# Kernel optimization log

Measured on AMD Instinct MI355X. Metric: run time of the kernel, lower is better.

The kernel has to match this reference:

```python
import jax, jax.numpy as jnp
import numpy as np

DIM = 24
HID = 256
N = 4096
NUM_LO = DIM * (DIM - 1) // 2  # 276
NEG = -0.01  # slope used in the hand-written Jacobians (source uses -0.01, NOT the fwd leaky slope 0.01; faithful)


def _linear_params(key, out_dim, in_dim):
    kw, kb = jax.random.split(key)
    s = 1.0 / np.sqrt(in_dim)
    W = jax.random.uniform(kw, (out_dim, in_dim), jnp.float32, -s, s)
    b = jax.random.uniform(kb, (out_dim,), jnp.float32, -s, s)
    return W, b


def setup_inputs() -> dict:
    key = jax.random.key(0)
    k = jax.random.split(key, 7)
    W1, b1 = _linear_params(k[0], HID, DIM)
    W2, b2 = _linear_params(k[1], HID, HID)
    WG, bG = _linear_params(k[2], DIM, HID)
    WLd, bLd = _linear_params(k[3], DIM, HID)
    WLo, bLo = _linear_params(k[4], NUM_LO, HID)
    q = jax.random.normal(k[5], (N, DIM), jnp.float32)
    q_dot = jax.random.normal(k[6], (N, DIM), jnp.float32)
    return {"q": q, "q_dot": q_dot, "W1": W1, "b1": b1, "W2": W2, "b2": b2,
            "WG": WG, "bG": bG, "WLd": WLd, "bLd": bLd, "WLo": WLo, "bLo": bLo}


def _forward(q, q_dot, W1, b1, W2, b2, WG, bG, WLd, bLd, WLo, bLo):
    n, d = q.shape
    tr, tc = np.tril_indices(d, -1)  # row-major strict-lower order == torch mask-flatten order
    di = np.arange(d)
    # MLP trunk (torch leaky_relu default slope 0.01)
    h1 = jax.nn.leaky_relu(q @ W1.T + b1)                       # [n,HID]
    h2 = jax.nn.leaky_relu(h1 @ W2.T + b2)                      # [n,HID]
    h3 = h2 @ WLd.T + bLd                                       # [n,d]
    g = h2 @ WG.T + bG                                          # [n,d]
    Ld = jax.nn.softplus(h3)                                    # [n,d]
    Lo = h2 @ WLo.T + bLo                                       # [n,NUM_LO]
    # Lower-triangular L (diag_embed(Ld) + masked strict-lower fill)
    L = jnp.zeros((n, d, d), q.dtype).at[:, tr, tc].set(Lo).at[:, di, di].set(Ld)
    # Hand-written Jacobian chain; diag_embed(v)@W == v[:,:,None]*W (direct elementwise scaling)
    dR1 = jnp.where(h1 > 0, 1.0, NEG)
    J1 = dR1[:, :, None] * W1                                    # dh1/dq  [n,HID,d]
    dR2 = jnp.where(h2 > 0, 1.0, NEG)
    J2 = dR2[:, :, None] * jnp.einsum('ij,njd->nid', W2, J1)     # dh2/dq  [n,HID,d]
    sig = jax.nn.sigmoid(h3)
    dld_dq = sig[:, :, None] * jnp.einsum('ij,njd->nid', WLd, J2)  # [n,d,d]
    dlo_dq = jnp.einsum('oj,njd->nod', WLo, J2)                  # [n,NUM_LO,d]
    dld_dt = jnp.einsum('nid,nd->ni', dld_dq, q_dot)             # [n,d]
    dlo_dt = jnp.einsum('nod,nd->no', dlo_dq, q_dot)             # [n,NUM_LO]
    dL_dt = jnp.zeros((n, d, d), q.dtype).at[:, tr, tc].set(dlo_dt).at[:, di, di].set(dld_dt)
    # 4D assembly: torch does L[L==1] = dlo_dq.view(-1), which reinterprets the (lo, q_idx)
    # flat buffer in (q_idx, tril_pos) order -> plain reshape replicates that exactly.
    vals = dlo_dq.reshape(n, d, NUM_LO)
    dld_dq_p = dld_dq.transpose(0, 2, 1)                         # [n, d_q, d_ld]
    dL_dq = jnp.zeros((n, d, d, d), q.dtype).at[:, :, tr, tc].set(vals).at[:, :, di, di].set(dld_dq_p)
    eye = jnp.eye(d, dtype=q.dtype)
    M = L @ L.transpose(0, 2, 1) + 1e-9 * eye
    dM_dt = L @ dL_dt.transpose(0, 2, 1) + dL_dt @ L.transpose(0, 2, 1)
    # Quadratic term. torch: q_dot.repeat(d,1)/L.repeat(d,1,1) index as (i % n) while
    # dL_dq.view(n*d,d,d) indexes as (i // d, i % d) -> replicate exactly (faithful).
    idx = jnp.arange(n * d) % n
    qd_r = q_dot[idx]                                            # [n*d, d]
    L_r = L[idx]                                                 # [n*d, d, d]
    dL_i = dL_dq.reshape(n * d, d, d)
    S = dL_i @ L_r.transpose(0, 2, 1) + L_r @ dL_i.transpose(0, 2, 1)
    quad = jnp.einsum('bi,bij,bj->b', qd_r, S, qd_r).reshape(n, d)
    c = jnp.einsum('nij,nj->ni', dM_dt, q_dot) - 0.5 * quad
    return M, c, g


def reference(q, q_dot, W1, b1, W2, b2, WG, bG, WLd, bLd, WLo, bLo):
    return _forward(q, q_dot, W1, b1, W2, b2, WG, bG, WLd, bLd, WLo, bLo)
```

## Files before the change

### kernel.cpp

```cpp
#include <hip/hip_runtime.h>
#include <math.h>

#define DIM 24
#define HID 256
#define NLO 276
#define NSAMP 4096
#define C_OFF 2359296
#define G_OFF 2457600

#define OFF_W2FH 0
#define OFF_W2FL 32768
#define OFF_WEFH 65536
#define OFF_WEFL 106496
#define OFF_W1H16 147456
#define OFF_W1L16 151552
#define OFF_W2H16 155648
#define OFF_W2L16 188416
#define OFF_WHH16 221184
#define OFF_WHL16 264192
#define OFF_REC  307200
#define REC_STRIDE 364

typedef __attribute__((ext_vector_type(8))) short bf16x8;
typedef __attribute__((ext_vector_type(8))) _Float16 f16x8;
typedef __attribute__((ext_vector_type(4))) float f32x4;

__device__ __forceinline__ float leaky(float x){ return x > 0.f ? x : 0.01f*x; }
__device__ __forceinline__ unsigned short f2b(float f){
  unsigned u = __float_as_uint(f);
  return (unsigned short)((u + 0x7FFFu + ((u >> 16) & 1u)) >> 16);
}
__device__ __forceinline__ float b2f(unsigned short h){ return __uint_as_float(((unsigned)h) << 16); }
__device__ __forceinline__ void f2h2(float v, unsigned short* hi, unsigned short* lo){
  _Float16 h = (_Float16)v;
  _Float16 l = (_Float16)((v - (float)h) * 4096.f);
  *hi = *(unsigned short*)&h; *lo = *(unsigned short*)&l;
}

__global__ __launch_bounds__(256) void k0_prep(
    const float* __restrict__ W1, const float* __restrict__ W2,
    const float* __restrict__ WG, const float* __restrict__ WLd,
    const float* __restrict__ WLo, float* __restrict__ ws)
{
  const int tid = blockIdx.x*256 + threadIdx.x;
  const int nth = gridDim.x*256;
  unsigned short* W2FH = (unsigned short*)(ws + OFF_W2FH);
  unsigned short* W2FL = (unsigned short*)(ws + OFF_W2FL);
  for (int e = tid; e < 65536; e += nth){
    int j=e&7, l=(e>>3)&63, kb=(e>>9)&7, mt=e>>12;
    int m = mt*16+(l&15), k = kb*32+((l>>4)&3)*8+j;
    float v = W2[m*256+k];
    unsigned short h = f2b(v);
    W2FH[e]=h; W2FL[e]=f2b(v-b2f(h));
  }
  unsigned short* WEFH = (unsigned short*)(ws + OFF_WEFH);
  unsigned short* WEFL = (unsigned short*)(ws + OFF_WEFL);
  for (int e = tid; e < 81920; e += nth){
    int j=e&7, l=(e>>3)&63, kb=(e>>9)&7, mt=e>>12;
    int r = mt*16+(l&15), k = kb*32+((l>>4)&3)*8+j;
    float v = 0.f;
    if (r < 24) v = WLd[r*256+k]; else if (r < 300) v = WLo[(r-24)*256+k];
    unsigned short h = f2b(v);
    WEFH[e]=h; WEFL[e]=f2b(v-b2f(h));
  }
  unsigned short* W1H = (unsigned short*)(ws + OFF_W1H16);
  unsigned short* W1L = (unsigned short*)(ws + OFF_W1L16);
  for (int e = tid; e < 8192; e += nth){
    int j=e&7, l=(e>>3)&63, mt=e>>9;
    int m = mt*16+(l&15), k = ((l>>4)&3)*8+j;
    float v = (k < 24) ? W1[m*24+k] : 0.f;
    f2h2(v, &W1H[e], &W1L[e]);
  }
  unsigned short* W2H = (unsigned short*)(ws + OFF_W2H16);
  unsigned short* W2L = (unsigned short*)(ws + OFF_W2L16);
  for (int e = tid; e < 65536; e += nth){
    int j=e&7, l=(e>>3)&63, kb=(e>>9)&7, mt=e>>12;
    int m = mt*16+(l&15), k = kb*32+((l>>4)&3)*8+j;
    f2h2(W2[m*256+k], &W2H[e], &W2L[e]);
  }
  unsigned short* WHH = (unsigned short*)(ws + OFF_WHH16);
  unsigned short* WHL = (unsigned short*)(ws + OFF_WHL16);
  for (int e = tid; e < 86016; e += nth){
    int j=e&7, l=(e>>3)&63, kb=(e>>9)&7, mt=e>>12;
    int rr = mt*16+(l&15), k = kb*32+((l>>4)&3)*8+j;
    float v = 0.f;
    if (rr < 24) v = WLd[rr*256+k];
    else if (rr < 48) v = WG[(rr-24)*256+k];
    else if (rr < 324) v = WLo[(rr-48)*256+k];
    f2h2(v, &WHH[e], &WHL[e]);
  }
}

__global__ __launch_bounds__(256) void k1_fwd(
    const float* __restrict__ q, const float* __restrict__ qd_g,
    const float* __restrict__ b1, const float* __restrict__ b2,
    const float* __restrict__ bG, const float* __restrict__ bLd,
    const float* __restrict__ bLo, float* __restrict__ ws,
    float* __restrict__ out)
{
  const int s0 = blockIdx.x*32, t = threadIdx.x;
  const int w = t>>6, l = t&63, l15 = l&15, l4g = (l>>4)&3;
  float* REC = ws + OFF_REC;

  __shared__ __align__(16) char pool[33792];
  __shared__ float qd_s[32][24];
  __shared__ float Ld_s[32][24];
  __shared__ unsigned char mb[32][64];
  unsigned short* BQH = (unsigned short*)pool;
  unsigned short* BQL = BQH + 1280;
  unsigned short* BH2 = (unsigned short*)pool;
  unsigned short* BL2 = BH2 + 8448;

  for (int f = t; f < 768; f += 256){
    float v = q[s0*24 + f];
    int n = f/24, k = f%24;
    f2h2(v, &BQH[n*40+k], &BQL[n*40+k]);
    ((float*)qd_s)[f] = qd_g[s0*24 + f];
  }
  { int n = t>>3, k = 24 + (t&7); BQH[n*40+k]=0; BQL[n*40+k]=0; }
  __syncthreads();

  f32x4 aH[4][2], aX[4][2];
  #pragma unroll
  for (int i=0;i<4;++i) for (int nt=0;nt<2;++nt){ aH[i][nt]=(f32x4){0,0,0,0}; aX[i][nt]=(f32x4){0,0,0,0}; }
  {
    const f16x8* WH = (const f16x8*)(ws + OFF_W1H16);
    const f16x8* WL = (const f16x8*)(ws + OFF_W1L16);
    f16x8 Af[4], Al[4], Bh[2], Bl[2];
    #pragma unroll
    for (int i=0;i<4;++i){ int mt=w+4*i; Af[i]=WH[mt*64+l]; Al[i]=WL[mt*64+l]; }
    #pragma unroll
    for (int nt=0;nt<2;++nt){
      int off=(nt*16+l15)*40 + l4g*8;
      Bh[nt]=*(const f16x8*)(BQH+off); Bl[nt]=*(const f16x8*)(BQL+off);
    }
    #pragma unroll
    for (int i=0;i<4;++i)
      #pragma unroll
      for (int nt=0;nt<2;++nt){
        aH[i][nt]=__builtin_amdgcn_mfma_f32_16x16x32_f16(Af[i],Bh[nt],aH[i][nt],0,0,0);
        aX[i][nt]=__builtin_amdgcn_mfma_f32_16x16x32_f16(Af[i],Bl[nt],aX[i][nt],0,0,0);
        aX[i][nt]=__builtin_amdgcn_mfma_f32_16x16x32_f16(Al[i],Bh[nt],aX[i][nt],0,0,0);
      }
  }
  __syncthreads();
  #pragma unroll
  for (int i=0;i<4;++i){
    int m0=(w+4*i)*16+4*l4g;
    float4 bb = *(const float4*)(b1+m0);
    #pragma unroll
    for (int nt=0;nt<2;++nt){
      int n = nt*16+l15;
      unsigned nib=0; unsigned short hs[4], ls[4];
      #pragma unroll
      for (int r=0;r<4;++r){
        float val = aH[i][nt][r] + aX[i][nt][r]*(1.f/4096.f) + ((const float*)&bb)[r];
        if (val > 0.f) nib |= 1u<<r;
        f2h2(leaky(val), &hs[r], &ls[r]);
      }
      mb[n][(m0>>2)] = (unsigned char)nib;
      *(uint2*)(BH2 + n*264 + m0) = make_uint2((unsigned)hs[0]|((unsigned)hs[1]<<16),
                                               (unsigned)hs[2]|((unsigned)hs[3]<<16));
      *(uint2*)(BL2 + n*264 + m0) = make_uint2((unsigned)ls[0]|((unsigned)ls[1]<<16),
                                               (unsigned)ls[2]|((unsigned)ls[3]<<16));
    }
  }
  __syncthreads();
  {
    int n = t>>3, w8 = t&7; unsigned word = 0;
    #pragma unroll
    for (int b=0;b<8;++b) word |= (unsigned)(mb[n][w8*8+b] & 0xFu) << (4*b);
    ((unsigned*)(REC + (size_t)(s0+n)*REC_STRIDE))[w8] = word;
  }

  #pragma unroll
  for (int i=0;i<4;++i) for (int nt=0;nt<2;++nt){ aH[i][nt]=(f32x4){0,0,0,0}; aX[i][nt]=(f32x4){0,0,0,0}; }
  {
    const f16x8* WH = (const f16x8*)(ws + OFF_W2H16);
    const f16x8* WL = (const f16x8*)(ws + OFF_W2L16);
    for (int kb=0;kb<8;++kb){
      f16x8 Af[4], Al[4], Bh[2], Bl[2];
      #pragma unroll
      for (int i=0;i<4;++i){ int mt=w+4*i; Af[i]=WH[(mt*8+kb)*64+l]; Al[i]=WL[(mt*8+kb)*64+l]; }
      #pragma unroll
      for (int nt=0;nt<2;++nt){
        int off=(nt*16+l15)*264 + kb*32 + l4g*8;
        Bh[nt]=*(const f16x8*)(BH2+off); Bl[nt]=*(const f16x8*)(BL2+off);
      }
      #pragma unroll
      for (int i=0;i<4;++i)
        #pragma unroll
        for (int nt=0;nt<2;++nt){
          aH[i][nt]=__builtin_amdgcn_mfma_f32_16x16x32_f16(Af[i],Bh[nt],aH[i][nt],0,0,0);
          aX[i][nt]=__builtin_amdgcn_mfma_f32_16x16x32_f16(Af[i],Bl[nt],aX[i][nt],0,0,0);
          aX[i][nt]=__builtin_amdgcn_mfma_f32_16x16x32_f16(Al[i],Bh[nt],aX[i][nt],0,0,0);
        }
    }
  }
  __syncthreads();
  #pragma unroll
  for (int i=0;i<4;++i){
    int m0=(w+4*i)*16+4*l4g;
    float4 bb = *(const float4*)(b2+m0);
    #pragma unroll
    for (int nt=0;nt<2;++nt){
      int n = nt*16+l15;
      unsigned nib=0; unsigned short hs[4], ls[4];
      #pragma unroll
      for (int r=0;r<4;++r){
        float val = aH[i][nt][r] + aX[i][nt][r]*(1.f/4096.f) + ((const float*)&bb)[r];
        if (val > 0.f) nib |= 1u<<r;
        f2h2(leaky(val), &hs[r], &ls[r]);
      }
      mb[n][(m0>>2)] = (unsigned char)nib;
      *(uint2*)(BH2 + n*264 + m0) = make_uint2((unsigned)hs[0]|((unsigned)hs[1]<<16),
                                               (unsigned)hs[2]|((unsigned)hs[3]<<16));
      *(uint2*)(BL2 + n*264 + m0) = make_uint2((unsigned)ls[0]|((unsigned)ls[1]<<16),
                                               (unsigned)ls[2]|((unsigned)ls[3]<<16));
    }
  }
  __syncthreads();
  {
    int n = t>>3, w8 = t&7; unsigned word = 0;
    #pragma unroll
    for (int b=0;b<8;++b) word |= (unsigned)(mb[n][w8*8+b] & 0xFu) << (4*b);
    ((unsigned*)(REC + (size_t)(s0+n)*REC_STRIDE))[8+w8] = word;
  }

  for (int pass=0; pass<2; ++pass){
    f32x4 cH[3][2], cX[3][2];
    #pragma unroll
    for (int i=0;i<3;++i) for (int nt=0;nt<2;++nt){ cH[i][nt]=(f32x4){0,0,0,0}; cX[i][nt]=(f32x4){0,0,0,0}; }
    const f16x8* WH = (const f16x8*)(ws + OFF_WHH16);
    const f16x8* WL = (const f16x8*)(ws + OFF_WHL16);
    for (int kb=0;kb<8;++kb){
      f16x8 Af[3], Al[3], Bh[2], Bl[2];
      #pragma unroll
      for (int i=0;i<3;++i){
        int mt = w + 4*(3*pass+i);
        if (mt < 21){ Af[i]=WH[(mt*8+kb)*64+l]; Al[i]=WL[(mt*8+kb)*64+l]; }
      }
      #pragma unroll
      for (int nt=0;nt<2;++nt){
        int off=(nt*16+l15)*264 + kb*32 + l4g*8;
        Bh[nt]=*(const f16x8*)(BH2+off); Bl[nt]=*(const f16x8*)(BL2+off);
      }
      #pragma unroll
      for (int i=0;i<3;++i){
        int mt = w + 4*(3*pass+i);
        if (mt < 21){
          #pragma unroll
          for (int nt=0;nt<2;++nt){
            cH[i][nt]=__builtin_amdgcn_mfma_f32_16x16x32_f16(Af[i],Bh[nt],cH[i][nt],0,0,0);
            cX[i][nt]=__builtin_amdgcn_mfma_f32_16x16x32_f16(Af[i],Bl[nt],cX[i][nt],0,0,0);
            cX[i][nt]=__builtin_amdgcn_mfma_f32_16x16x32_f16(Al[i],Bh[nt],cX[i][nt],0,0,0);
          }
        }
      }
    }
    #pragma unroll
    for (int i=0;i<3;++i){
      int mt = w + 4*(3*pass+i);
      if (mt >= 21) continue;
      int m0 = mt*16+4*l4g;
      #pragma unroll
      for (int nt=0;nt<2;++nt){
        int n = nt*16+l15, sG = s0+n;
        float* recn = REC + (size_t)sG*REC_STRIDE;
        #pragma unroll
        for (int r=0;r<4;++r){
          int rr = m0+r;
          float val = cH[i][nt][r] + cX[i][nt][r]*(1.f/4096.f);
          if (rr < 24){
            val += bLd[rr];
            recn[16+rr] = 1.f/(1.f + expf(-val));
            float sp = fmaxf(val,0.f) + log1pf(expf(-fabsf(val)));
            recn[64+rr] = sp; Ld_s[n][rr] = sp;
          } else if (rr < 48){
            out[G_OFF + sG*24 + (rr-24)] = val + bG[rr-24];
          } else if (rr < 324){
            recn[88 + rr-48] = val + bLo[rr-48];
          }
        }
      }
    }
  }
  __syncthreads();

  for (int task=t; task<768; task+=256){
    int n = task/24, c = task%24;
    float* recn = REC + (size_t)(s0+n)*REC_STRIDE;
    float u = qd_s[n][c]*Ld_s[n][c];
    for (int r=c+1; r<24; ++r) u += qd_s[n][r]*recn[88 + r*(r-1)/2 + c];
    recn[40+c] = u;
  }
}

__global__ __launch_bounds__(256, 2) void k2_jac(
    const float* __restrict__ q_dot, const float* __restrict__ W1g,
    float* __restrict__ ws, float* __restrict__ out)
{
  const int n0 = blockIdx.x*2, t = threadIdx.x;
  const int w = t >> 6, l = t & 63;
  const int l15 = l & 15, l4g = (l >> 4) & 3;
  float* REC = ws + OFF_REC;

  __shared__ __align__(16) char pool[58176];
  __shared__ float dld2v[1200];
  __shared__ float qd2[2][24], u2[2][24], sig2[2][24], dld_dt2[2][24], w12[2][24];
  __shared__ unsigned msk[2][16];
  float* Lp = (float*)pool;
  unsigned short* BH = (unsigned short*)pool;
  unsigned short* BL = BH + 12672;
  float* dlo2 = (float*)pool;
  float* dlo_dt2 = (float*)(pool + 55200);
  float* qp = (float*)(pool + 57408);

  if (t < 32) msk[t>>4][t&15] = ((const unsigned*)(REC + (size_t)(n0+(t>>4))*REC_STRIDE))[t&15];
  if (t < 48){
    int s = t/24, i = t%24;
    const float* rc = REC + (size_t)(n0+s)*REC_STRIDE;
    sig2[s][i] = rc[16+i]; u2[s][i] = rc[40+i]; qd2[s][i] = q_dot[(n0+s)*24+i];
  }
  for (int e = t; e < 1152; e += 256){
    int s = e/576, rc = e%576, r = rc/24, c = rc%24;
    const float* rr = REC + (size_t)(n0+s)*REC_STRIDE;
    float v = 0.f;
    if (r == c) v = rr[64+r]; else if (r > c) v = rr[88 + r*(r-1)/2 + c];
    Lp[s*600 + r*25 + c] = v;
  }
  __syncthreads();
  for (int e = t; e < 1152; e += 256){
    int s = e/576, rc = e%576, r = rc/24, c = rc%24, km = min(r,c);
    float acc = (r == c) ? 1e-9f : 0.f;
    const float* Ls = Lp + s*600;
    for (int k = 0; k <= km; ++k) acc += Ls[r*25+k]*Ls[c*25+k];
    out[(size_t)(n0+s)*576 + rc] = acc;
  }
  __syncthreads();

  {
    float w1r[24];
    #pragma unroll
    for (int d = 0; d < 24; ++d) w1r[d] = W1g[t*24 + d];
    float dr0 = ((msk[0][t>>5] >> (t&31)) & 1u) ? 1.f : -0.01f;
    float dr1 = ((msk[1][t>>5] >> (t&31)) & 1u) ? 1.f : -0.01f;
    #pragma unroll
    for (int c = 0; c < 48; ++c){
      int s = c >= 24, d = c - 24*s;
      float f = (s ? dr1 : dr0) * w1r[d];
      unsigned short h = f2b(f);
      BH[c*264 + t] = h;
      BL[c*264 + t] = f2b(f - b2f(h));
    }
  }
  __syncthreads();

  f32x4 accD[4][3];
  #pragma unroll
  for (int i = 0; i < 4; ++i)
    #pragma unroll
    for (int nt = 0; nt < 3; ++nt) accD[i][nt] = (f32x4){0.f,0.f,0.f,0.f};
  {
    const bf16x8* AHp = (const bf16x8*)(ws + OFF_W2FH);
    const bf16x8* ALp = (const bf16x8*)(ws + OFF_W2FL);
    for (int kb = 0; kb < 8; ++kb){
      bf16x8 AH[4], AL[4], BHf[3], BLf[3];
      #pragma unroll
      for (int i = 0; i < 4; ++i){
        int mt = 4*w + i;
        AH[i] = AHp[(mt*8+kb)*64 + l];
        AL[i] = ALp[(mt*8+kb)*64 + l];
      }
      #pragma unroll
      for (int nt = 0; nt < 3; ++nt){
        int off = (nt*16 + l15)*264 + kb*32 + l4g*8;
        BHf[nt] = *(const bf16x8*)(BH + off);
        BLf[nt] = *(const bf16x8*)(BL + off);
      }
      #pragma unroll
      for (int i = 0; i < 4; ++i)
        #pragma unroll
        for (int nt = 0; nt < 3; ++nt){
          accD[i][nt] = __builtin_amdgcn_mfma_f32_16x16x32_bf16(AH[i], BHf[nt], accD[i][nt], 0, 0, 0);
          accD[i][nt] = __builtin_amdgcn_mfma_f32_16x16x32_bf16(AH[i], BLf[nt], accD[i][nt], 0, 0, 0);
          accD[i][nt] = __builtin_amdgcn_mfma_f32_16x16x32_bf16(AL[i], BHf[nt], accD[i][nt], 0, 0, 0);
        }
    }
  }
  __syncthreads();

  {
    #pragma unroll
    for (int i = 0; i < 4; ++i){
      int mt = 4*w + i;
      int m0 = mt*16 + 4*l4g;
      int bb = m0 & 31;
      #pragma unroll
      for (int nt = 0; nt < 3; ++nt){
        int c = nt*16 + l15;
        int s = c >= 24;
        unsigned word = msk[s][8 + (mt>>1)];
        unsigned short hs[4], ls[4];
        #pragma unroll
        for (int r = 0; r < 4; ++r){
          float sc = ((word >> (bb + r)) & 1u) ? 1.f : -0.01f;
          float v = sc * accD[i][nt][r];
          hs[r] = f2b(v); ls[r] = f2b(v - b2f(hs[r]));
        }
        *(uint2*)(BH + c*264 + m0) = make_uint2((unsigned)hs[0] | ((unsigned)hs[1]<<16),
                                                (unsigned)hs[2] | ((unsigned)hs[3]<<16));
        *(uint2*)(BL + c*264 + m0) = make_uint2((unsigned)ls[0] | ((unsigned)ls[1]<<16),
                                                (unsigned)ls[2] | ((unsigned)ls[3]<<16));
      }
    }
  }
  __syncthreads();

  f32x4 accE[5][3];
  #pragma unroll
  for (int i = 0; i < 5; ++i)
    #pragma unroll
    for (int nt = 0; nt < 3; ++nt) accE[i][nt] = (f32x4){0.f,0.f,0.f,0.f};
  {
    const bf16x8* AHp = (const bf16x8*)(ws + OFF_WEFH);
    const bf16x8* ALp = (const bf16x8*)(ws + OFF_WEFL);
    for (int kb = 0; kb < 8; ++kb){
      bf16x8 AH[5], AL[5], BHf[3], BLf[3];
      #pragma unroll
      for (int i = 0; i < 5; ++i){
        int mt = 5*w + i;
        AH[i] = AHp[(mt*8+kb)*64 + l];
        AL[i] = ALp[(mt*8+kb)*64 + l];
      }
      #pragma unroll
      for (int nt = 0; nt < 3; ++nt){
        int off = (nt*16 + l15)*264 + kb*32 + l4g*8;
        BHf[nt] = *(const bf16x8*)(BH + off);
        BLf[nt] = *(const bf16x8*)(BL + off);
      }
      #pragma unroll
      for (int i = 0; i < 5; ++i)
        #pragma unroll
        for (int nt = 0; nt < 3; ++nt){
          accE[i][nt] = __builtin_amdgcn_mfma_f32_16x16x32_bf16(AH[i], BHf[nt], accE[i][nt], 0, 0, 0);
          accE[i][nt] = __builtin_amdgcn_mfma_f32_16x16x32_bf16(AH[i], BLf[nt], accE[i][nt], 0, 0, 0);
          accE[i][nt] = __builtin_amdgcn_mfma_f32_16x16x32_bf16(AL[i], BHf[nt], accE[i][nt], 0, 0, 0);
        }
    }
  }
  __syncthreads();

  #pragma unroll
  for (int i = 0; i < 5; ++i){
    int mt = 5*w + i;
    #pragma unroll
    for (int nt = 0; nt < 3; ++nt){
      int c = nt*16 + l15;
      int s = c >= 24, d = c - 24*s;
      #pragma unroll
      for (int r = 0; r < 4; ++r){
        int re = mt*16 + 4*l4g + r;
        float v = accE[i][nt][r];
        if (re < 24) dld2v[s*600 + re*25 + d] = sig2[s][re]*v;
        else if (re < 300) dlo2[s*6900 + (re-24)*25 + d] = v;
      }
    }
  }
  __syncthreads();

  for (int o2 = t; o2 < 552; o2 += 256){
    int s = o2/276, o = o2%276;
    float a = 0.f;
    #pragma unroll
    for (int d = 0; d < 24; ++d) a += dlo2[s*6900 + o*25 + d]*qd2[s][d];
    dlo_dt2[s*276 + o] = a;
  }
  if (t < 48){
    int s = t/24, i = t%24;
    float a = 0.f;
    #pragma unroll
    for (int d = 0; d < 24; ++d) a += dld2v[s*600 + i*25 + d]*qd2[s][d];
    dld_dt2[s][i] = a;
  }
  __syncthreads();

  if (t < 192){
    int g = t/48, si = t%48, s = si/24, i = si%24;
    int n = n0 + s;
    int m = (n*24 + i) & (NSAMP-1);
    const float* qdm = q_dot + m*24;
    const float* um  = REC + (size_t)m*REC_STRIDE + 40;
    float part = 0.f;
    for (int c2 = g; c2 < 24; c2 += 4){
      float v = qdm[c2]*dld2v[s*600 + c2*25 + i];
      for (int r = c2+1; r < 24; ++r){
        int f = i*276 + r*(r-1)/2 + c2;
        v += qdm[r]*dlo2[s*6900 + (f/24)*25 + (f%24)];
      }
      part += um[c2]*v;
    }
    qp[g*48 + si] = part;
  }
  if (t < 48){
    int s = t/24, i = t%24;
    float a = qd2[s][i]*dld_dt2[s][i];
    for (int j = i+1; j < 24; ++j) a += qd2[s][j]*dlo_dt2[s*276 + j*(j-1)/2 + i];
    w12[s][i] = a;
  }
  __syncthreads();

  if (t < 48){
    int s = t/24, i = t%24, n = n0 + s;
    const float* recn = REC + (size_t)n*REC_STRIDE;
    float cs = 0.f;
    for (int k = 0; k < i; ++k){
      float Lik = recn[88 + i*(i-1)/2 + k];
      cs += Lik*w12[s][k] + dlo_dt2[s*276 + i*(i-1)/2 + k]*u2[s][k];
    }
    cs += recn[64+i]*w12[s][i] + dld_dt2[s][i]*u2[s][i];
    float quad = qp[t] + qp[48+t] + qp[96+t] + qp[144+t];
    out[C_OFF + n*24 + i] = cs - quad;
  }
}

extern "C" void kernel_launch(void* const* d_in, const int* in_sizes, int n_in,
                              void* d_out, int out_size, void* d_ws, size_t ws_size,
                              hipStream_t stream)
{
  const float* q   = (const float*)d_in[0];
  const float* qd  = (const float*)d_in[1];
  const float* W1  = (const float*)d_in[2];
  const float* b1  = (const float*)d_in[3];
  const float* W2  = (const float*)d_in[4];
  const float* b2  = (const float*)d_in[5];
  const float* WG  = (const float*)d_in[6];
  const float* bG  = (const float*)d_in[7];
  const float* WLd = (const float*)d_in[8];
  const float* bLd = (const float*)d_in[9];
  const float* WLo = (const float*)d_in[10];
  const float* bLo = (const float*)d_in[11];
  float* out = (float*)d_out;
  float* ws  = (float*)d_ws;

  k0_prep<<<256, 256, 0, stream>>>(W1, W2, WG, WLd, WLo, ws);
  k1_fwd<<<NSAMP/32, 256, 0, stream>>>(q, qd, b1, b2, bG, bLd, bLo, ws, out);
  k2_jac<<<NSAMP/2, 256, 0, stream>>>(qd, W1, ws, out);
}
```

Measured before the change: 290.7 us.

## Split Jacobian kernel into MFMA and tail kernels with transposed workspace

Per-sample records are replaced with feature-major (transposed) arrays so that k1 writes are coalesced. The Jacobian kernel becomes two kernels: kDE runs only the MFMA chain and spills the 300x24 dL/dq block per sample to a global buffer, with less shared memory and a higher occupancy bound. kT then does the M product, time derivatives and quadratic term with one block per sample. The split is meant to raise MFMA occupancy and parallelise the scalar tail, at the cost of a large global round trip and extra launches that are chunked by workspace size.

```diff
diff --git a/kernel.cpp b/kernel.cpp
--- a/kernel.cpp
+++ b/kernel.cpp
@@ -18,8 +18,12 @@
 #define OFF_W2L16 188416
 #define OFF_WHH16 221184
 #define OFF_WHL16 264192
-#define OFF_REC  307200
-#define REC_STRIDE 364
+#define OFF_MSKT 307200
+#define OFF_SIGT 372736
+#define OFF_LDT  471040
+#define OFF_UT   569344
+#define OFF_LOT  667648
+#define OFF_EBUF 1798144
 
 typedef __attribute__((ext_vector_type(8))) short bf16x8;
 typedef __attribute__((ext_vector_type(8))) _Float16 f16x8;
@@ -100,7 +104,11 @@
 {
   const int s0 = blockIdx.x*32, t = threadIdx.x;
   const int w = t>>6, l = t&63, l15 = l&15, l4g = (l>>4)&3;
-  float* REC = ws + OFF_REC;
+  unsigned* MSKT = (unsigned*)(ws + OFF_MSKT);
+  float* SIGT = ws + OFF_SIGT;
+  float* LDT  = ws + OFF_LDT;
+  float* UT   = ws + OFF_UT;
+  float* LOT  = ws + OFF_LOT;
 
   __shared__ __align__(16) char pool[33792];
   __shared__ float qd_s[32][24];
@@ -167,10 +175,10 @@
   }
   __syncthreads();
   {
-    int n = t>>3, w8 = t&7; unsigned word = 0;
+    int n = t&31, w8 = t>>5; unsigned word = 0;
     #pragma unroll
     for (int b=0;b<8;++b) word |= (unsigned)(mb[n][w8*8+b] & 0xFu) << (4*b);
-    ((unsigned*)(REC + (size_t)(s0+n)*REC_STRIDE))[w8] = word;
+    MSKT[w8*NSAMP + s0+n] = word;
   }
 
   #pragma unroll
@@ -221,10 +229,10 @@
   }
   __syncthreads();
   {
-    int n = t>>3, w8 = t&7; unsigned word = 0;
+    int n = t&31, w8 = t>>5; unsigned word = 0;
     #pragma unroll
     for (int b=0;b<8;++b) word |= (unsigned)(mb[n][w8*8+b] & 0xFu) << (4*b);
-    ((unsigned*)(REC + (size_t)(s0+n)*REC_STRIDE))[8+w8] = word;
+    MSKT[(8+w8)*NSAMP + s0+n] = word;
   }
 
   for (int pass=0; pass<2; ++pass){
@@ -266,20 +274,19 @@
       #pragma unroll
       for (int nt=0;nt<2;++nt){
         int n = nt*16+l15, sG = s0+n;
-        float* recn = REC + (size_t)sG*REC_STRIDE;
         #pragma unroll
         for (int r=0;r<4;++r){
           int rr = m0+r;
           float val = cH[i][nt][r] + cX[i][nt][r]*(1.f/4096.f);
           if (rr < 24){
             val += bLd[rr];
-            recn[16+rr] = 1.f/(1.f + expf(-val));
+            SIGT[rr*NSAMP + sG] = 1.f/(1.f + expf(-val));
             float sp = fmaxf(val,0.f) + log1pf(expf(-fabsf(val)));
-            recn[64+rr] = sp; Ld_s[n][rr] = sp;
+            LDT[rr*NSAMP + sG] = sp; Ld_s[n][rr] = sp;
           } else if (rr < 48){
             out[G_OFF + sG*24 + (rr-24)] = val + bG[rr-24];
           } else if (rr < 324){
-            recn[88 + rr-48] = val + bLo[rr-48];
+            LOT[(rr-48)*NSAMP + sG] = val + bLo[rr-48];
           }
         }
       }
@@ -287,56 +294,30 @@
   }
   __syncthreads();
 
-  for (int task=t; task<768; task+=256){
-    int n = task/24, c = task%24;
-    float* recn = REC + (size_t)(s0+n)*REC_STRIDE;
-    float u = qd_s[n][c]*Ld_s[n][c];
-    for (int r=c+1; r<24; ++r) u += qd_s[n][r]*recn[88 + r*(r-1)/2 + c];
-    recn[40+c] = u;
-  }
-}
-
-__global__ __launch_bounds__(256, 2) void k2_jac(
-    const float* __restrict__ q_dot, const float* __restrict__ W1g,
-    float* __restrict__ ws, float* __restrict__ out)
+  {
+    int n = t&31, c = t>>5;
+    for (; c < 24; c += 8){
+      float u = qd_s[n][c]*Ld_s[n][c];
+      for (int r=c+1; r<24; ++r) u += qd_s[n][r]*LOT[(r*(r-1)/2 + c)*NSAMP + s0+n];
+      UT[c*NSAMP + s0+n] = u;
+    }
+  }
+}
+
+__global__ __launch_bounds__(256, 3) void kDE(
+    const float* __restrict__ W1g, float* __restrict__ ws,
+    float* __restrict__ Ebuf, int base)
 {
-  const int n0 = blockIdx.x*2, t = threadIdx.x;
+  const int n0 = base + blockIdx.x*2, t = threadIdx.x;
   const int w = t >> 6, l = t & 63;
   const int l15 = l & 15, l4g = (l >> 4) & 3;
-  float* REC = ws + OFF_REC;
-
-  __shared__ __align__(16) char pool[58176];
-  __shared__ float dld2v[1200];
-  __shared__ float qd2[2][24], u2[2][24], sig2[2][24], dld_dt2[2][24], w12[2][24];
+  const unsigned* MSKT = (const unsigned*)(ws + OFF_MSKT);
+
+  __shared__ __align__(16) unsigned short BH[48*264];
+  __shared__ __align__(16) unsigned short BL[48*264];
   __shared__ unsigned msk[2][16];
-  float* Lp = (float*)pool;
-  unsigned short* BH = (unsigned short*)pool;
-  unsigned short* BL = BH + 12672;
-  float* dlo2 = (float*)pool;
-  float* dlo_dt2 = (float*)(pool + 55200);
-  float* qp = (float*)(pool + 57408);
-
-  if (t < 32) msk[t>>4][t&15] = ((const unsigned*)(REC + (size_t)(n0+(t>>4))*REC_STRIDE))[t&15];
-  if (t < 48){
-    int s = t/24, i = t%24;
-    const float* rc = REC + (size_t)(n0+s)*REC_STRIDE;
-    sig2[s][i] = rc[16+i]; u2[s][i] = rc[40+i]; qd2[s][i] = q_dot[(n0+s)*24+i];
-  }
-  for (int e = t; e < 1152; e += 256){
-    int s = e/576, rc = e%576, r = rc/24, c = rc%24;
-    const float* rr = REC + (size_t)(n0+s)*REC_STRIDE;
-    float v = 0.f;
-    if (r == c) v = rr[64+r]; else if (r > c) v = rr[88 + r*(r-1)/2 + c];
-    Lp[s*600 + r*25 + c] = v;
-  }
-  __syncthreads();
-  for (int e = t; e < 1152; e += 256){
-    int s = e/576, rc = e%576, r = rc/24, c = rc%24, km = min(r,c);
-    float acc = (r == c) ? 1e-9f : 0.f;
-    const float* Ls = Lp + s*600;
-    for (int k = 0; k <= km; ++k) acc += Ls[r*25+k]*Ls[c*25+k];
-    out[(size_t)(n0+s)*576 + rc] = acc;
-  }
+
+  if (t < 32) msk[t>>4][t&15] = MSKT[(t&15)*NSAMP + n0 + (t>>4)];
   __syncthreads();
 
   {
@@ -390,29 +371,27 @@
   }
   __syncthreads();
 
-  {
-    #pragma unroll
-    for (int i = 0; i < 4; ++i){
-      int mt = 4*w + i;
-      int m0 = mt*16 + 4*l4g;
-      int bb = m0 & 31;
-      #pragma unroll
-      for (int nt = 0; nt < 3; ++nt){
-        int c = nt*16 + l15;
-        int s = c >= 24;
-        unsigned word = msk[s][8 + (mt>>1)];
-        unsigned short hs[4], ls[4];
-        #pragma unroll
-        for (int r = 0; r < 4; ++r){
-          float sc = ((word >> (bb + r)) & 1u) ? 1.f : -0.01f;
-          float v = sc * accD[i][nt][r];
-          hs[r] = f2b(v); ls[r] = f2b(v - b2f(hs[r]));
-        }
-        *(uint2*)(BH + c*264 + m0) = make_uint2((unsigned)hs[0] | ((unsigned)hs[1]<<16),
-                                                (unsigned)hs[2] | ((unsigned)hs[3]<<16));
-        *(uint2*)(BL + c*264 + m0) = make_uint2((unsigned)ls[0] | ((unsigned)ls[1]<<16),
-                                                (unsigned)ls[2] | ((unsigned)ls[3]<<16));
-      }
+  #pragma unroll
+  for (int i = 0; i < 4; ++i){
+    int mt = 4*w + i;
+    int m0 = mt*16 + 4*l4g;
+    int bb = m0 & 31;
+    #pragma unroll
+    for (int nt = 0; nt < 3; ++nt){
+      int c = nt*16 + l15;
+      int s = c >= 24;
+      unsigned word = msk[s][8 + (mt>>1)];
+      unsigned short hs[4], ls[4];
+      #pragma unroll
+      for (int r = 0; r < 4; ++r){
+        float sc = ((word >> (bb + r)) & 1u) ? 1.f : -0.01f;
+        float v = sc * accD[i][nt][r];
+        hs[r] = f2b(v); ls[r] = f2b(v - b2f(hs[r]));
+      }
+      *(uint2*)(BH + c*264 + m0) = make_uint2((unsigned)hs[0] | ((unsigned)hs[1]<<16),
+                                              (unsigned)hs[2] | ((unsigned)hs[3]<<16));
+      *(uint2*)(BL + c*264 + m0) = make_uint2((unsigned)ls[0] | ((unsigned)ls[1]<<16),
+                                              (unsigned)ls[2] | ((unsigned)ls[3]<<16));
     }
   }
   __syncthreads();
@@ -449,7 +428,6 @@
         }
     }
   }
-  __syncthreads();
 
   #pragma unroll
   for (int i = 0; i < 5; ++i){
@@ -458,68 +436,91 @@
     for (int nt = 0; nt < 3; ++nt){
       int c = nt*16 + l15;
       int s = c >= 24, d = c - 24*s;
+      float* eb = Ebuf + (size_t)(blockIdx.x*2 + s)*7200;
       #pragma unroll
       for (int r = 0; r < 4; ++r){
         int re = mt*16 + 4*l4g + r;
-        float v = accE[i][nt][r];
-        if (re < 24) dld2v[s*600 + re*25 + d] = sig2[s][re]*v;
-        else if (re < 300) dlo2[s*6900 + (re-24)*25 + d] = v;
-      }
-    }
-  }
-  __syncthreads();
-
-  for (int o2 = t; o2 < 552; o2 += 256){
-    int s = o2/276, o = o2%276;
+        if (re < 300) eb[re*24 + d] = accE[i][nt][r];
+      }
+    }
+  }
+}
+
+__global__ __launch_bounds__(256) void kT(
+    const float* __restrict__ q_dot, const float* __restrict__ ws_c,
+    const float* __restrict__ Ebuf, int base, float* __restrict__ out)
+{
+  const int n = base + blockIdx.x, t = threadIdx.x;
+  const float* SIGT = ws_c + OFF_SIGT;
+  const float* LDT  = ws_c + OFF_LDT;
+  const float* UT   = ws_c + OFF_UT;
+  const float* LOT  = ws_c + OFF_LOT;
+  const float* eb   = Ebuf + (size_t)blockIdx.x*7200;
+
+  __shared__ float Lp[600];
+  __shared__ float qp[192];
+  __shared__ float dt_lo[276], dt_ld[24];
+  __shared__ float sig_s[24], qd_s[24], u_s[24], w1_s[24];
+
+  if (t < 24){
+    sig_s[t] = SIGT[t*NSAMP + n];
+    qd_s[t]  = q_dot[n*24 + t];
+    u_s[t]   = UT[t*NSAMP + n];
+  }
+  for (int e = t; e < 600; e += 256) Lp[e] = 0.f;
+  __syncthreads();
+  if (t < 24) Lp[t*25 + t] = LDT[t*NSAMP + n];
+  for (int p = t; p < 276; p += 256){
+    int r = (int)((1.f + sqrtf(1.f + 8.f*(float)p))*0.5f);
+    while (r*(r-1)/2 > p) --r;
+    while ((r+1)*r/2 <= p) ++r;
+    int c = p - r*(r-1)/2;
+    Lp[r*25 + c] = LOT[p*NSAMP + n];
+  }
+  __syncthreads();
+
+  for (int e = t; e < 576; e += 256){
+    int r = e/24, c = e%24, km = min(r,c);
+    float acc = (r == c) ? 1e-9f : 0.f;
+    for (int k = 0; k <= km; ++k) acc += Lp[r*25+k]*Lp[c*25+k];
+    out[(size_t)n*576 + e] = acc;
+  }
+  for (int rr = t; rr < 300; rr += 256){
     float a = 0.f;
     #pragma unroll
-    for (int d = 0; d < 24; ++d) a += dlo2[s*6900 + o*25 + d]*qd2[s][d];
-    dlo_dt2[s*276 + o] = a;
-  }
-  if (t < 48){
-    int s = t/24, i = t%24;
-    float a = 0.f;
-    #pragma unroll
-    for (int d = 0; d < 24; ++d) a += dld2v[s*600 + i*25 + d]*qd2[s][d];
-    dld_dt2[s][i] = a;
-  }
-  __syncthreads();
-
+    for (int d = 0; d < 24; ++d) a += eb[rr*24 + d]*qd_s[d];
+    if (rr < 24) dt_ld[rr] = sig_s[rr]*a; else dt_lo[rr-24] = a;
+  }
   if (t < 192){
-    int g = t/48, si = t%48, s = si/24, i = si%24;
-    int n = n0 + s;
+    int i = t % 24, g = t / 24;
     int m = (n*24 + i) & (NSAMP-1);
     const float* qdm = q_dot + m*24;
-    const float* um  = REC + (size_t)m*REC_STRIDE + 40;
     float part = 0.f;
-    for (int c2 = g; c2 < 24; c2 += 4){
-      float v = qdm[c2]*dld2v[s*600 + c2*25 + i];
-      for (int r = c2+1; r < 24; ++r){
-        int f = i*276 + r*(r-1)/2 + c2;
-        v += qdm[r]*dlo2[s*6900 + (f/24)*25 + (f%24)];
-      }
-      part += um[c2]*v;
-    }
-    qp[g*48 + si] = part;
-  }
-  if (t < 48){
-    int s = t/24, i = t%24;
-    float a = qd2[s][i]*dld_dt2[s][i];
-    for (int j = i+1; j < 24; ++j) a += qd2[s][j]*dlo_dt2[s*276 + j*(j-1)/2 + i];
-    w12[s][i] = a;
-  }
-  __syncthreads();
-
-  if (t < 48){
-    int s = t/24, i = t%24, n = n0 + s;
-    const float* recn = REC + (size_t)n*REC_STRIDE;
+    for (int c2 = g; c2 < 24; c2 += 8){
+      float v = qdm[c2]*sig_s[c2]*eb[c2*24 + i];
+      for (int r = c2+1; r < 24; ++r)
+        v += qdm[r]*eb[576 + i*276 + r*(r-1)/2 + c2];
+      part += UT[c2*NSAMP + m]*v;
+    }
+    qp[g*24 + i] = part;
+  }
+  __syncthreads();
+  if (t < 24){
+    int i = t;
+    float a = qd_s[i]*dt_ld[i];
+    for (int j = i+1; j < 24; ++j) a += qd_s[j]*dt_lo[j*(j-1)/2 + i];
+    w1_s[i] = a;
+  }
+  __syncthreads();
+  if (t < 24){
+    int i = t;
     float cs = 0.f;
-    for (int k = 0; k < i; ++k){
-      float Lik = recn[88 + i*(i-1)/2 + k];
-      cs += Lik*w12[s][k] + dlo_dt2[s*276 + i*(i-1)/2 + k]*u2[s][k];
-    }
-    cs += recn[64+i]*w12[s][i] + dld_dt2[s][i]*u2[s][i];
-    float quad = qp[t] + qp[48+t] + qp[96+t] + qp[144+t];
+    for (int k = 0; k < i; ++k)
+      cs += Lp[i*25+k]*w1_s[k] + dt_lo[i*(i-1)/2 + k]*u_s[k];
+    cs += Lp[i*25+i]*w1_s[i] + dt_ld[i]*u_s[i];
+    float quad = 0.f;
+    #pragma unroll
+    for (int g = 0; g < 8; ++g) quad += qp[g*24 + i];
     out[C_OFF + n*24 + i] = cs - quad;
   }
 }
@@ -542,8 +543,19 @@
   const float* bLo = (const float*)d_in[11];
   float* out = (float*)d_out;
   float* ws  = (float*)d_ws;
+  float* Ebuf = ws + OFF_EBUF;
 
   k0_prep<<<256, 256, 0, stream>>>(W1, W2, WG, WLd, WLo, ws);
   k1_fwd<<<NSAMP/32, 256, 0, stream>>>(q, qd, b1, b2, bG, bLd, bLo, ws, out);
-  k2_jac<<<NSAMP/2, 256, 0, stream>>>(qd, W1, ws, out);
-}
+
+  long avail = (long)(ws_size/4) - OFF_EBUF;
+  int chunk = (int)(avail / 7200);
+  if (chunk > NSAMP) chunk = NSAMP;
+  chunk &= ~1;
+  if (chunk < 2) chunk = 2;
+  for (int bse = 0; bse < NSAMP; bse += chunk){
+    int cur = NSAMP - bse < chunk ? NSAMP - bse : chunk;
+    kDE<<<cur/2, 256, 0, stream>>>(W1, ws, Ebuf, bse);
+    kT <<<cur,   256, 0, stream>>>(qd, ws, Ebuf, bse, out);
+  }
+}
```

Measured after the change: 353.1 us. +21.5%, slower.
